# Performance work log

Hardware: AMD Instinct MI355X
Metric: run time of the kernel (lower is better)

## Reference

```python
import jax, jax.numpy as jnp
import numpy as np

B, SQ, SC, D = 16, 1024, 1024, 768
H = 2 * D  # 1536, fc width
NCLS = 2


def setup_inputs() -> dict:
    key = jax.random.key(0)
    ks = jax.random.split(key, 8)
    q = jax.random.normal(ks[0], (B, SQ, D), jnp.float32)
    c = jax.random.normal(ks[1], (B, SC, D), jnp.float32)
    mask_q = jax.random.randint(ks[2], (B, SQ), 0, 2).astype(jnp.int32)
    mask_c = jax.random.randint(ks[3], (B, SC), 0, 2).astype(jnp.int32)
    labels = jax.random.randint(ks[4], (B,), 0, NCLS)
    # torch nn.Linear convention: weight [out, in], y = x @ W.T + b
    W1 = jax.random.normal(ks[5], (H, H), jnp.float32) * 0.02
    b1 = jnp.zeros((H,), jnp.float32)
    W2 = jax.random.normal(ks[6], (NCLS, H), jnp.float32) * 0.02
    b2 = jnp.zeros((NCLS,), jnp.float32)
    return dict(q=q, c=c, mask_q=mask_q, mask_c=mask_c, labels=labels,
                W1=W1, b1=b1, W2=W2, b2=b2)


def reference(q, c, mask_q, mask_c, labels, W1, b1, W2, b2):
    # masked QK^T score matrix: [B, SQ, SC]
    s = jnp.einsum('bik,bjk->bij', q, c)
    s = s * mask_q[:, :, None].astype(s.dtype) * mask_c[:, None, :].astype(s.dtype)
    s = jnp.where(s == 0.0, -jnp.inf, s)  # x[x == 0.0] = -inf
    p = jnp.nan_to_num(jax.nn.softmax(s, axis=2))   # softmax over context axis
    pp = jnp.nan_to_num(jax.nn.softmax(s, axis=1))  # softmax over question axis
    a = jnp.einsum('bjk,bij->bk', c, p)   # weighted combine into context feats
    bb = jnp.einsum('bik,bij->bk', q, pp)  # weighted combine into question feats
    x = jnp.concatenate([a, bb], axis=1)  # [B, 1536]
    x = jnp.tanh(x @ W1.T + b1)           # fc1 + tanh (dropout = identity in eval)
    logits = x @ W2.T + b2                # fc2
    logp = jax.nn.log_softmax(logits, axis=1)  # LogSoftmax(dim=1)
    # NLLLoss (mean reduction)
    loss = -jnp.mean(jnp.take_along_axis(logp, labels[:, None], axis=1))
    return (loss, logp)
```

## Files before the change

### kernel.cpp

```cpp
#include <hip/hip_runtime.h>
#include <math.h>

#define B_   16
#define SQ_  1024
#define SC_  1024
#define D_   768
#define H_   1536
#define BK   32
#define LDK  40

typedef __attribute__((ext_vector_type(4))) float f32x4;
typedef __attribute__((ext_vector_type(8))) short bf16x8;

__device__ __forceinline__ unsigned cvtpk(float x, float y) {
  unsigned r;
  asm("v_cvt_pk_bf16_f32 %0, %1, %2" : "=v"(r) : "v"(x), "v"(y));
  return r;
}

__device__ __forceinline__ void split4(float4 v, uint2& hi, uint2& lo) {
  unsigned h01 = cvtpk(v.x, v.y);
  unsigned h23 = cvtpk(v.z, v.w);
  float h0 = __uint_as_float(h01 << 16);
  float h1 = __uint_as_float(h01 & 0xFFFF0000u);
  float h2 = __uint_as_float(h23 << 16);
  float h3 = __uint_as_float(h23 & 0xFFFF0000u);
  hi = make_uint2(h01, h23);
  lo = make_uint2(cvtpk(v.x - h0, v.y - h1), cvtpk(v.z - h2, v.w - h3));
}

__device__ __forceinline__ double exp_pos(float s) {
  float t = s * 1.4426950408889634f;
  float n = floorf(t);
  float p = exp2f(t - n);
  long long e = (long long)n;
  double scale = __longlong_as_double((unsigned long long)(e + 1023LL) << 52);
  return (double)p * scale;
}

__global__ __launch_bounds__(256) void compact_kernel(
    const int* __restrict__ mask_q, const int* __restrict__ mask_c,
    int* __restrict__ idx_q, int* __restrict__ idx_c, int* __restrict__ cnt)
{
  int which = blockIdx.x & 1;
  int b     = blockIdx.x >> 1;
  const int* m = (which ? mask_c : mask_q) + b * 1024;
  int* idx     = (which ? idx_c : idx_q) + b * 1024;

  __shared__ int tsum[256];
  int t = threadIdx.x;
  int v[4], s = 0;
#pragma unroll
  for (int e = 0; e < 4; ++e) { v[e] = (m[t * 4 + e] != 0) ? 1 : 0; s += v[e]; }
  tsum[t] = s;
  __syncthreads();
  for (int off = 1; off < 256; off <<= 1) {
    int add = (t >= off) ? tsum[t - off] : 0;
    __syncthreads();
    tsum[t] += add;
    __syncthreads();
  }
  int pos = tsum[t] - s;
#pragma unroll
  for (int e = 0; e < 4; ++e) {
    if (v[e]) idx[pos++] = t * 4 + e;
  }
  if (t == 255) cnt[b * 2 + which] = tsum[255];
}

__global__ void tile_setup_kernel(const int* __restrict__ cnt, int* __restrict__ tmeta)
{
  if (threadIdx.x == 0) {
    int off = 0;
    for (int b = 0; b < B_; ++b) {
      int ntq = (cnt[2 * b] + 63) >> 6;
      int ntc = (cnt[2 * b + 1] + 63) >> 6;
      tmeta[1 + b]  = off;
      tmeta[17 + b] = ntc;
      off += ntq * ntc;
    }
    tmeta[0]  = off;
    tmeta[33] = 0;
  }
}

__global__ __launch_bounds__(256) void gemm_mfma_kernel(
    const float* __restrict__ q, const float* __restrict__ c,
    const int* __restrict__ idx_q, const int* __restrict__ idx_c,
    const int* __restrict__ cnt, int* __restrict__ tmeta,
    float* __restrict__ S, double* __restrict__ R, double* __restrict__ C)
{
  __shared__ unsigned short Ah[2][64][LDK];
  __shared__ unsigned short Al[2][64][LDK];
  __shared__ unsigned short Bh[2][64][LDK];
  __shared__ unsigned short Bl[2][64][LDK];
  __shared__ int tidx_s;

  const int t    = threadIdx.x;
  const int lane = t & 63;
  const int w    = t >> 6;
  const int srow = t >> 2;
  const int kc   = (t & 3) * 4;
  const int fr   = lane & 15;
  const int fq   = lane >> 4;
  const int kg   = fq * 8;

  const int total = tmeta[0];

  while (true) {
    if (t == 0) tidx_s = atomicAdd(&tmeta[33], 1);
    __syncthreads();
    const int idx = tidx_s;
    if (idx >= total) break;

    int bb = 0;
#pragma unroll
    for (int k = 1; k < 16; ++k) bb += (idx >= tmeta[1 + k]) ? 1 : 0;
    const int rem = idx - tmeta[1 + bb];
    const int ntc = tmeta[17 + bb];
    const int ty  = rem / ntc;
    const int tx  = rem - ty * ntc;
    const int i0  = ty * 64, j0 = tx * 64;
    const int nq  = cnt[2 * bb], nc = cnt[2 * bb + 1];

    const int rq = idx_q[bb * 1024 + min(i0 + srow, nq - 1)];
    const int rc = idx_c[bb * 1024 + min(j0 + srow, nc - 1)];
    const float* qrowP = q + ((size_t)bb * SQ_ + rq) * D_;
    const float* crowP = c + ((size_t)bb * SC_ + rc) * D_;

    f32x4 acc[4] = {};

    float4 av0 = *(const float4*)(qrowP + kc);
    float4 av1 = *(const float4*)(qrowP + kc + 16);
    float4 bv0 = *(const float4*)(crowP + kc);
    float4 bv1 = *(const float4*)(crowP + kc + 16);
    {
      uint2 hi, lo;
      split4(av0, hi, lo); *(uint2*)&Ah[0][srow][kc]      = hi; *(uint2*)&Al[0][srow][kc]      = lo;
      split4(av1, hi, lo); *(uint2*)&Ah[0][srow][kc + 16] = hi; *(uint2*)&Al[0][srow][kc + 16] = lo;
      split4(bv0, hi, lo); *(uint2*)&Bh[0][srow][kc]      = hi; *(uint2*)&Bl[0][srow][kc]      = lo;
      split4(bv1, hi, lo); *(uint2*)&Bh[0][srow][kc + 16] = hi; *(uint2*)&Bl[0][srow][kc + 16] = lo;
    }
    __syncthreads();

    int cur = 0;
    for (int k0 = 0; k0 < D_; k0 += BK) {
      const int next = k0 + BK;
      const bool has_next = (next < D_);
      if (has_next) {
        av0 = *(const float4*)(qrowP + next + kc);
        av1 = *(const float4*)(qrowP + next + kc + 16);
        bv0 = *(const float4*)(crowP + next + kc);
        bv1 = *(const float4*)(crowP + next + kc + 16);
      }

      bf16x8 b_h = *reinterpret_cast<const bf16x8*>(&Bh[cur][w * 16 + fr][kg]);
      bf16x8 b_l = *reinterpret_cast<const bf16x8*>(&Bl[cur][w * 16 + fr][kg]);
#pragma unroll
      for (int m = 0; m < 4; ++m) {
        bf16x8 a_h = *reinterpret_cast<const bf16x8*>(&Ah[cur][m * 16 + fr][kg]);
        bf16x8 a_l = *reinterpret_cast<const bf16x8*>(&Al[cur][m * 16 + fr][kg]);
        acc[m] = __builtin_amdgcn_mfma_f32_16x16x32_bf16(a_h, b_h, acc[m], 0, 0, 0);
        acc[m] = __builtin_amdgcn_mfma_f32_16x16x32_bf16(a_h, b_l, acc[m], 0, 0, 0);
        acc[m] = __builtin_amdgcn_mfma_f32_16x16x32_bf16(a_l, b_h, acc[m], 0, 0, 0);
      }

      if (has_next) {
        int nxt = cur ^ 1;
        uint2 hi, lo;
        split4(av0, hi, lo); *(uint2*)&Ah[nxt][srow][kc]      = hi; *(uint2*)&Al[nxt][srow][kc]      = lo;
        split4(av1, hi, lo); *(uint2*)&Ah[nxt][srow][kc + 16] = hi; *(uint2*)&Al[nxt][srow][kc + 16] = lo;
        split4(bv0, hi, lo); *(uint2*)&Bh[nxt][srow][kc]      = hi; *(uint2*)&Bl[nxt][srow][kc]      = lo;
        split4(bv1, hi, lo); *(uint2*)&Bh[nxt][srow][kc + 16] = hi; *(uint2*)&Bl[nxt][srow][kc + 16] = lo;
      }
      __syncthreads();
      cur ^= 1;
    }

    double* rowAcc = reinterpret_cast<double*>(&Ah[0][0][0]);
    const int col = j0 + w * 16 + fr;
    const bool cok = (col < nc);
    double colSum = 0.0;
#pragma unroll
    for (int m = 0; m < 4; ++m) {
      int rbase = i0 + m * 16 + fq * 4;
      float* Sp = S + ((size_t)bb * SQ_ + rbase) * SC_ + col;
#pragma unroll
      for (int rr = 0; rr < 4; ++rr) {
        float v = acc[m][rr];
        bool valid = ((rbase + rr) < nq) && cok && (v != 0.f);
        Sp[(size_t)rr * SC_] = valid ? v : -INFINITY;
        double e = valid ? exp_pos(v) : 0.0;
        colSum += e;
        double rsum = e;
        rsum += __shfl_xor(rsum, 1);
        rsum += __shfl_xor(rsum, 2);
        rsum += __shfl_xor(rsum, 4);
        rsum += __shfl_xor(rsum, 8);
        if (fr == 0) rowAcc[w * 64 + m * 16 + fq * 4 + rr] = rsum;
      }
    }
    colSum += __shfl_xor(colSum, 16);
    colSum += __shfl_xor(colSum, 32);
    if (fq == 0 && cok) atomicAdd(&C[bb * SC_ + col], colSum);
    __syncthreads();
    if (t < 64) {
      double rs = rowAcc[t] + rowAcc[64 + t] + rowAcc[128 + t] + rowAcc[192 + t];
      if ((i0 + t) < nq && rs != 0.0) atomicAdd(&R[bb * SQ_ + i0 + t], rs);
    }
    __syncthreads();
  }
}

__global__ __launch_bounds__(1024) void pass2_kernel(
    const float* __restrict__ S, const int* __restrict__ cnt,
    const double* __restrict__ R, const double* __restrict__ C,
    float* __restrict__ cp, float* __restrict__ rpp)
{
  __shared__ float lnR_lds[SQ_];
  __shared__ float red[16][64];

  int b  = blockIdx.y;
  int j0 = blockIdx.x * 64;
  int nq_pad = (cnt[2 * b] + 63) & ~63;
  int nc_pad = (cnt[2 * b + 1] + 63) & ~63;
  if (j0 >= nc_pad) return;
  int t = threadIdx.x;

  if (t < nq_pad) {
    double Ri = R[b * SQ_ + t];
    lnR_lds[t] = (Ri > 0.0) ? (float)log(Ri) : INFINITY;
  }
  __syncthreads();

  int lane = t & 63, wv = t >> 6;
  int j = j0 + lane;
  double Cj = C[b * SC_ + j];
  float lnCj = (Cj > 0.0) ? (float)log(Cj) : INFINITY;

  int chunk = nq_pad >> 4;
  int i0 = wv * chunk;
  const float* Sb = S + ((size_t)b * SQ_ + i0) * SC_ + j;

  float cpAcc = 0.f;
  for (int ii = 0; ii < chunk; ++ii) {
    int i = i0 + ii;
    float v = Sb[(size_t)ii * SC_];
    cpAcc += __expf(v - lnR_lds[i]);
    float e2 = __expf(v - lnCj);
#pragma unroll
    for (int o = 32; o; o >>= 1) e2 += __shfl_xor(e2, o);
    if (lane == 0) atomicAdd(&rpp[b * SQ_ + i], e2);
  }

  red[wv][lane] = cpAcc;
  __syncthreads();
  if (t < 64) {
    float s = 0.f;
#pragma unroll
    for (int k = 0; k < 16; ++k) s += red[k][t];
    cp[b * SC_ + j0 + t] = s;
  }
}

__global__ __launch_bounds__(256) void combine_kernel(
    const float* __restrict__ q, const float* __restrict__ c,
    const int* __restrict__ idx_q, const int* __restrict__ idx_c,
    const int* __restrict__ cnt,
    const float* __restrict__ cp, const float* __restrict__ rpp,
    float* __restrict__ X)
{
  int jc = blockIdx.x;
  int op = blockIdx.y;
  int b  = blockIdx.z;
  int t  = threadIdx.x;

  int n = op ? cnt[2 * b] : cnt[2 * b + 1];
  const float* src = op ? (q + (size_t)b * SQ_ * D_) : (c + (size_t)b * SC_ * D_);
  const float* wv  = op ? (rpp + b * SQ_) : (cp + b * SC_);
  const int*   idx = (op ? idx_q : idx_c) + b * 1024;

  float a0 = 0.f, a1 = 0.f, a2 = 0.f;
  int je = min(jc * 32 + 32, n);
  for (int j = jc * 32; j < je; ++j) {
    float wj = wv[j];
    const float* r = src + (size_t)idx[j] * D_;
    a0 += wj * r[t];
    a1 += wj * r[t + 256];
    a2 += wj * r[t + 512];
  }
  float* xp = X + (size_t)b * H_ + op * D_;
  atomicAdd(&xp[t], a0);
  atomicAdd(&xp[t + 256], a1);
  atomicAdd(&xp[t + 512], a2);
}

__global__ __launch_bounds__(256) void fc1_kernel(
    const float* __restrict__ X, const float* __restrict__ W1,
    const float* __restrict__ b1, float* __restrict__ Y)
{
  int w = threadIdx.x >> 6, lane = threadIdx.x & 63;
  int h = blockIdx.x * 4 + w;
  const float4* wr = (const float4*)(W1 + (size_t)h * H_);
  float4 wv[6];
#pragma unroll
  for (int it = 0; it < 6; ++it) wv[it] = wr[it * 64 + lane];
  float bias = b1[h];

  for (int b = 0; b < B_; ++b) {
    const float4* x = (const float4*)(X + (size_t)b * H_);
    float accv = 0.f;
#pragma unroll
    for (int it = 0; it < 6; ++it) {
      float4 xv = x[it * 64 + lane];
      accv += xv.x * wv[it].x + xv.y * wv[it].y + xv.z * wv[it].z + xv.w * wv[it].w;
    }
#pragma unroll
    for (int o = 32; o; o >>= 1) accv += __shfl_xor(accv, o);
    if (lane == 0) Y[(size_t)b * H_ + h] = tanhf(accv + bias);
  }
}

__global__ __launch_bounds__(64) void fc2_loss_kernel(
    const float* __restrict__ Y, const float* __restrict__ W2,
    const float* __restrict__ b2, const int* __restrict__ labels,
    float* __restrict__ out)
{
  __shared__ float logp_s[B_][2];
  int t = threadIdx.x;
  if (t < 2 * B_) {
    int b = t >> 1, n = t & 1;
    const float* y = Y + (size_t)b * H_;
    const float* w = W2 + (size_t)n * H_;
    float accv = b2[n];
    for (int k = 0; k < H_; ++k) accv += y[k] * w[k];
    logp_s[b][n] = accv;
  }
  __syncthreads();
  if (t < B_) {
    float l0 = logp_s[t][0], l1 = logp_s[t][1];
    float m = fmaxf(l0, l1);
    float lse = m + logf(expf(l0 - m) + expf(l1 - m));
    logp_s[t][0] = l0 - lse;
    logp_s[t][1] = l1 - lse;
  }
  __syncthreads();
  if (t < 2 * B_) out[1 + t] = logp_s[t >> 1][t & 1];
  if (t == 0) {
    float loss = 0.f;
    for (int b = 0; b < B_; ++b) loss -= logp_s[b][labels[b]];
    out[0] = loss / (float)B_;
  }
}

extern "C" void kernel_launch(void* const* d_in, const int* in_sizes, int n_in,
                              void* d_out, int out_size, void* d_ws, size_t ws_size,
                              hipStream_t stream) {
  const float* q      = (const float*)d_in[0];
  const float* c      = (const float*)d_in[1];
  const int*   mask_q = (const int*)d_in[2];
  const int*   mask_c = (const int*)d_in[3];
  const int*   labels = (const int*)d_in[4];
  const float* W1     = (const float*)d_in[5];
  const float* b1     = (const float*)d_in[6];
  const float* W2     = (const float*)d_in[7];
  const float* b2     = (const float*)d_in[8];
  float* out = (float*)d_out;

  float*  ws   = (float*)d_ws;
  float*  S    = ws;
  double* R    = (double*)(ws + (size_t)B_ * SQ_ * SC_);
  double* C    = R + B_ * SQ_;
  float*  cp   = (float*)(C + B_ * SC_);
  float*  rpp  = cp + B_ * SC_;
  int*    cnt  = (int*)(rpp + B_ * SQ_);
  int*    tmeta = cnt + 2 * B_;
  int*    idx_q = tmeta + 34;
  int*    idx_c = idx_q + B_ * SQ_;
  float*  X    = ws;
  float*  Y    = ws + B_ * H_;

  (void)hipMemsetAsync((void*)R, 0, (size_t)(2 * B_ * SQ_) * sizeof(double)
                              + (size_t)(2 * B_ * SC_) * sizeof(float), stream);

  compact_kernel<<<2 * B_, 256, 0, stream>>>(mask_q, mask_c, idx_q, idx_c, cnt);
  tile_setup_kernel<<<1, 64, 0, stream>>>(cnt, tmeta);

  gemm_mfma_kernel<<<1024, 256, 0, stream>>>(q, c, idx_q, idx_c, cnt, tmeta, S, R, C);

  pass2_kernel<<<dim3(SC_ / 64, B_), 1024, 0, stream>>>(S, cnt, R, C, cp, rpp);

  (void)hipMemsetAsync((void*)X, 0, (size_t)B_ * H_ * sizeof(float), stream);
  combine_kernel<<<dim3(32, 2, B_), 256, 0, stream>>>(q, c, idx_q, idx_c, cnt,
                                                      cp, rpp, X);
  fc1_kernel<<<H_ / 4, 256, 0, stream>>>(X, W1, b1, Y);
  fc2_loss_kernel<<<1, 64, 0, stream>>>(Y, W2, b2, labels, out);
}
```

Baseline: 164.0 us.

## Replace LDS-staged persistent GEMM with register-direct 128x128 tiles per block

The score GEMM now drops shared-memory staging and the atomic persistent tile queue. Each block covers a 128x128 tile with four waves of 64x64 each, and every lane loads its MFMA fragments straight from global memory, splits them into bf16 hi/lo in registers and accumulates a 4x4 grid of MFMA tiles. Row and column exp-sums are reduced in registers before the atomics. This removes LDS traffic and __syncthreads at the cost of heavy register pressure, strided uncoalesced global loads, and a launch grid that now depends on tmeta. The host launch code (not shown) must size the grid to match.

```diff
diff --git a/kernel.cpp b/kernel.cpp
--- a/kernel.cpp
+++ b/kernel.cpp
@@ -6,8 +6,6 @@
 #define SC_  1024
 #define D_   768
 #define H_   1536
-#define BK   32
-#define LDK  40
 
 typedef __attribute__((ext_vector_type(4))) float f32x4;
 typedef __attribute__((ext_vector_type(8))) short bf16x8;
@@ -18,15 +16,22 @@
   return r;
 }
 
-__device__ __forceinline__ void split4(float4 v, uint2& hi, uint2& lo) {
-  unsigned h01 = cvtpk(v.x, v.y);
-  unsigned h23 = cvtpk(v.z, v.w);
-  float h0 = __uint_as_float(h01 << 16);
-  float h1 = __uint_as_float(h01 & 0xFFFF0000u);
-  float h2 = __uint_as_float(h23 << 16);
-  float h3 = __uint_as_float(h23 & 0xFFFF0000u);
-  hi = make_uint2(h01, h23);
-  lo = make_uint2(cvtpk(v.x - h0, v.y - h1), cvtpk(v.z - h2, v.w - h3));
+__device__ __forceinline__ void split8(float4 r0, float4 r1, bf16x8& h8, bf16x8& l8) {
+  unsigned h01 = cvtpk(r0.x, r0.y);
+  unsigned h23 = cvtpk(r0.z, r0.w);
+  unsigned h45 = cvtpk(r1.x, r1.y);
+  unsigned h67 = cvtpk(r1.z, r1.w);
+  float f0 = __uint_as_float(h01 << 16), f1 = __uint_as_float(h01 & 0xFFFF0000u);
+  float f2 = __uint_as_float(h23 << 16), f3 = __uint_as_float(h23 & 0xFFFF0000u);
+  float f4 = __uint_as_float(h45 << 16), f5 = __uint_as_float(h45 & 0xFFFF0000u);
+  float f6 = __uint_as_float(h67 << 16), f7 = __uint_as_float(h67 & 0xFFFF0000u);
+  unsigned l01 = cvtpk(r0.x - f0, r0.y - f1);
+  unsigned l23 = cvtpk(r0.z - f2, r0.w - f3);
+  unsigned l45 = cvtpk(r1.x - f4, r1.y - f5);
+  unsigned l67 = cvtpk(r1.z - f6, r1.w - f7);
+  union U { unsigned u[4]; bf16x8 v; };
+  U H; H.u[0] = h01; H.u[1] = h23; H.u[2] = h45; H.u[3] = h67; h8 = H.v;
+  U L; L.u[0] = l01; L.u[1] = l23; L.u[2] = l45; L.u[3] = l67; l8 = L.v;
 }
 
 __device__ __forceinline__ double exp_pos(float s) {
@@ -73,142 +78,152 @@
   if (threadIdx.x == 0) {
     int off = 0;
     for (int b = 0; b < B_; ++b) {
-      int ntq = (cnt[2 * b] + 63) >> 6;
-      int ntc = (cnt[2 * b + 1] + 63) >> 6;
+      int ntq = (cnt[2 * b] + 127) >> 7;
+      int ntc = (cnt[2 * b + 1] + 127) >> 7;
       tmeta[1 + b]  = off;
       tmeta[17 + b] = ntc;
       off += ntq * ntc;
     }
-    tmeta[0]  = off;
-    tmeta[33] = 0;
-  }
-}
-
-__global__ __launch_bounds__(256) void gemm_mfma_kernel(
+    tmeta[0] = off;
+  }
+}
+
+__global__ __launch_bounds__(256, 1) void gemm_mfma_kernel(
     const float* __restrict__ q, const float* __restrict__ c,
     const int* __restrict__ idx_q, const int* __restrict__ idx_c,
-    const int* __restrict__ cnt, int* __restrict__ tmeta,
+    const int* __restrict__ cnt, const int* __restrict__ tmeta,
     float* __restrict__ S, double* __restrict__ R, double* __restrict__ C)
 {
-  __shared__ unsigned short Ah[2][64][LDK];
-  __shared__ unsigned short Al[2][64][LDK];
-  __shared__ unsigned short Bh[2][64][LDK];
-  __shared__ unsigned short Bl[2][64][LDK];
-  __shared__ int tidx_s;
+  const int flat  = blockIdx.x;
+  const int total = tmeta[0];
+  if (flat >= total) return;
 
   const int t    = threadIdx.x;
   const int lane = t & 63;
   const int w    = t >> 6;
-  const int srow = t >> 2;
-  const int kc   = (t & 3) * 4;
-  const int fr   = lane & 15;
-  const int fq   = lane >> 4;
-  const int kg   = fq * 8;
-
-  const int total = tmeta[0];
-
-  while (true) {
-    if (t == 0) tidx_s = atomicAdd(&tmeta[33], 1);
-    __syncthreads();
-    const int idx = tidx_s;
-    if (idx >= total) break;
-
-    int bb = 0;
-#pragma unroll
-    for (int k = 1; k < 16; ++k) bb += (idx >= tmeta[1 + k]) ? 1 : 0;
-    const int rem = idx - tmeta[1 + bb];
-    const int ntc = tmeta[17 + bb];
-    const int ty  = rem / ntc;
-    const int tx  = rem - ty * ntc;
-    const int i0  = ty * 64, j0 = tx * 64;
-    const int nq  = cnt[2 * bb], nc = cnt[2 * bb + 1];
-
-    const int rq = idx_q[bb * 1024 + min(i0 + srow, nq - 1)];
-    const int rc = idx_c[bb * 1024 + min(j0 + srow, nc - 1)];
-    const float* qrowP = q + ((size_t)bb * SQ_ + rq) * D_;
-    const float* crowP = c + ((size_t)bb * SC_ + rc) * D_;
-
-    f32x4 acc[4] = {};
-
-    float4 av0 = *(const float4*)(qrowP + kc);
-    float4 av1 = *(const float4*)(qrowP + kc + 16);
-    float4 bv0 = *(const float4*)(crowP + kc);
-    float4 bv1 = *(const float4*)(crowP + kc + 16);
-    {
-      uint2 hi, lo;
-      split4(av0, hi, lo); *(uint2*)&Ah[0][srow][kc]      = hi; *(uint2*)&Al[0][srow][kc]      = lo;
-      split4(av1, hi, lo); *(uint2*)&Ah[0][srow][kc + 16] = hi; *(uint2*)&Al[0][srow][kc + 16] = lo;
-      split4(bv0, hi, lo); *(uint2*)&Bh[0][srow][kc]      = hi; *(uint2*)&Bl[0][srow][kc]      = lo;
-      split4(bv1, hi, lo); *(uint2*)&Bh[0][srow][kc + 16] = hi; *(uint2*)&Bl[0][srow][kc + 16] = lo;
+
+  int bb = 0;
+#pragma unroll
+  for (int k = 1; k < 16; ++k) bb += (flat >= tmeta[1 + k]) ? 1 : 0;
+  const int rem = flat - tmeta[1 + bb];
+  const int ntc = tmeta[17 + bb];
+  const int ty  = rem / ntc;
+  const int tx  = rem - ty * ntc;
+  const int nq  = cnt[2 * bb], nc = cnt[2 * bb + 1];
+
+  const int i0 = ty * 128 + (w >> 1) * 64;
+  const int j0 = tx * 128 + (w & 1) * 64;
+  if (i0 >= nq || j0 >= nc) return;
+
+  const int fr = lane & 15;
+  const int fq = lane >> 4;
+
+  const float* aP[4];
+  const float* bP[4];
+#pragma unroll
+  for (int m = 0; m < 4; ++m) {
+    int r = idx_q[bb * 1024 + min(i0 + m * 16 + fr, nq - 1)];
+    aP[m] = q + ((size_t)bb * SQ_ + r) * D_ + fq * 8;
+  }
+#pragma unroll
+  for (int n = 0; n < 4; ++n) {
+    int cc = idx_c[bb * 1024 + min(j0 + n * 16 + fr, nc - 1)];
+    bP[n] = c + ((size_t)bb * SC_ + cc) * D_ + fq * 8;
+  }
+
+  f32x4 acc[4][4] = {};
+  float4 aRaw[4][2], bRaw[4][2];
+#pragma unroll
+  for (int m = 0; m < 4; ++m) {
+    aRaw[m][0] = *(const float4*)(aP[m]);
+    aRaw[m][1] = *(const float4*)(aP[m] + 4);
+  }
+#pragma unroll
+  for (int n = 0; n < 4; ++n) {
+    bRaw[n][0] = *(const float4*)(bP[n]);
+    bRaw[n][1] = *(const float4*)(bP[n] + 4);
+  }
+
+  for (int k0 = 0; k0 < D_; k0 += 32) {
+    bf16x8 aH[4], aL[4], bH[4], bL[4];
+#pragma unroll
+    for (int m = 0; m < 4; ++m) split8(aRaw[m][0], aRaw[m][1], aH[m], aL[m]);
+#pragma unroll
+    for (int n = 0; n < 4; ++n) split8(bRaw[n][0], bRaw[n][1], bH[n], bL[n]);
+
+    const int nk = k0 + 32;
+    if (nk < D_) {
+#pragma unroll
+      for (int m = 0; m < 4; ++m) {
+        aRaw[m][0] = *(const float4*)(aP[m] + nk);
+        aRaw[m][1] = *(const float4*)(aP[m] + nk + 4);
+      }
+#pragma unroll
+      for (int n = 0; n < 4; ++n) {
+        bRaw[n][0] = *(const float4*)(bP[n] + nk);
+        bRaw[n][1] = *(const float4*)(bP[n] + nk + 4);
+      }
     }
-    __syncthreads();
-
-    int cur = 0;
-    for (int k0 = 0; k0 < D_; k0 += BK) {
-      const int next = k0 + BK;
-      const bool has_next = (next < D_);
-      if (has_next) {
-        av0 = *(const float4*)(qrowP + next + kc);
-        av1 = *(const float4*)(qrowP + next + kc + 16);
-        bv0 = *(const float4*)(crowP + next + kc);
-        bv1 = *(const float4*)(crowP + next + kc + 16);
+
+#pragma unroll
+    for (int n = 0; n < 4; ++n)
+#pragma unroll
+      for (int m = 0; m < 4; ++m) {
+        acc[m][n] = __builtin_amdgcn_mfma_f32_16x16x32_bf16(aH[m], bH[n], acc[m][n], 0, 0, 0);
+        acc[m][n] = __builtin_amdgcn_mfma_f32_16x16x32_bf16(aH[m], bL[n], acc[m][n], 0, 0, 0);
+        acc[m][n] = __builtin_amdgcn_mfma_f32_16x16x32_bf16(aL[m], bH[n], acc[m][n], 0, 0, 0);
       }
-
-      bf16x8 b_h = *reinterpret_cast<const bf16x8*>(&Bh[cur][w * 16 + fr][kg]);
-      bf16x8 b_l = *reinterpret_cast<const bf16x8*>(&Bl[cur][w * 16 + fr][kg]);
-#pragma unroll
-      for (int m = 0; m < 4; ++m) {
-        bf16x8 a_h = *reinterpret_cast<const bf16x8*>(&Ah[cur][m * 16 + fr][kg]);
-        bf16x8 a_l = *reinterpret_cast<const bf16x8*>(&Al[cur][m * 16 + fr][kg]);
-        acc[m] = __builtin_amdgcn_mfma_f32_16x16x32_bf16(a_h, b_h, acc[m], 0, 0, 0);
-        acc[m] = __builtin_amdgcn_mfma_f32_16x16x32_bf16(a_h, b_l, acc[m], 0, 0, 0);
-        acc[m] = __builtin_amdgcn_mfma_f32_16x16x32_bf16(a_l, b_h, acc[m], 0, 0, 0);
-      }
-
-      if (has_next) {
-        int nxt = cur ^ 1;
-        uint2 hi, lo;
-        split4(av0, hi, lo); *(uint2*)&Ah[nxt][srow][kc]      = hi; *(uint2*)&Al[nxt][srow][kc]      = lo;
-        split4(av1, hi, lo); *(uint2*)&Ah[nxt][srow][kc + 16] = hi; *(uint2*)&Al[nxt][srow][kc + 16] = lo;
-        split4(bv0, hi, lo); *(uint2*)&Bh[nxt][srow][kc]      = hi; *(uint2*)&Bl[nxt][srow][kc]      = lo;
-        split4(bv1, hi, lo); *(uint2*)&Bh[nxt][srow][kc + 16] = hi; *(uint2*)&Bl[nxt][srow][kc + 16] = lo;
-      }
-      __syncthreads();
-      cur ^= 1;
-    }
-
-    double* rowAcc = reinterpret_cast<double*>(&Ah[0][0][0]);
-    const int col = j0 + w * 16 + fr;
-    const bool cok = (col < nc);
-    double colSum = 0.0;
-#pragma unroll
-    for (int m = 0; m < 4; ++m) {
-      int rbase = i0 + m * 16 + fq * 4;
+  }
+
+  double rowPart[4][4];
+#pragma unroll
+  for (int m = 0; m < 4; ++m)
+#pragma unroll
+    for (int rr = 0; rr < 4; ++rr) rowPart[m][rr] = 0.0;
+  double colSum[4] = {0.0, 0.0, 0.0, 0.0};
+
+#pragma unroll
+  for (int m = 0; m < 4; ++m) {
+    const int rbase = i0 + m * 16 + fq * 4;
+#pragma unroll
+    for (int n = 0; n < 4; ++n) {
+      const int col = j0 + n * 16 + fr;
+      const bool cok = (col < nc);
       float* Sp = S + ((size_t)bb * SQ_ + rbase) * SC_ + col;
 #pragma unroll
       for (int rr = 0; rr < 4; ++rr) {
-        float v = acc[m][rr];
+        float v = acc[m][n][rr];
         bool valid = ((rbase + rr) < nq) && cok && (v != 0.f);
         Sp[(size_t)rr * SC_] = valid ? v : -INFINITY;
         double e = valid ? exp_pos(v) : 0.0;
-        colSum += e;
-        double rsum = e;
-        rsum += __shfl_xor(rsum, 1);
-        rsum += __shfl_xor(rsum, 2);
-        rsum += __shfl_xor(rsum, 4);
-        rsum += __shfl_xor(rsum, 8);
-        if (fr == 0) rowAcc[w * 64 + m * 16 + fq * 4 + rr] = rsum;
+        colSum[n] += e;
+        rowPart[m][rr] += e;
       }
     }
-    colSum += __shfl_xor(colSum, 16);
-    colSum += __shfl_xor(colSum, 32);
-    if (fq == 0 && cok) atomicAdd(&C[bb * SC_ + col], colSum);
-    __syncthreads();
-    if (t < 64) {
-      double rs = rowAcc[t] + rowAcc[64 + t] + rowAcc[128 + t] + rowAcc[192 + t];
-      if ((i0 + t) < nq && rs != 0.0) atomicAdd(&R[bb * SQ_ + i0 + t], rs);
+  }
+#pragma unroll
+  for (int m = 0; m < 4; ++m)
+#pragma unroll
+    for (int rr = 0; rr < 4; ++rr) {
+      double x = rowPart[m][rr];
+      x += __shfl_xor(x, 1); x += __shfl_xor(x, 2);
+      x += __shfl_xor(x, 4); x += __shfl_xor(x, 8);
+      rowPart[m][rr] = x;
     }
-    __syncthreads();
+  if (fr == 0) {
+#pragma unroll
+    for (int m = 0; m < 4; ++m)
+#pragma unroll
+      for (int rr = 0; rr < 4; ++rr) {
+        double x = rowPart[m][rr];
+        if (x != 0.0) atomicAdd(&R[bb * SQ_ + i0 + m * 16 + fq * 4 + rr], x);
+      }
+  }
+#pragma unroll
+  for (int n = 0; n < 4; ++n) {
+    double x = colSum[n];
+    x += __shfl_xor(x, 16); x += __shfl_xor(x, 32);
+    if (fq == 0 && x != 0.0) atomicAdd(&C[bb * SC_ + j0 + n * 16 + fr], x);
   }
 }
 
```

Result: slower. 203.2 us (+23.9%).

## Fold memsets into compact kernel and replace persistent tile scheduler with 3D grid

Applied to the files above, without the earlier changes.

Zeroing of the R/C/cp/rpp accumulators and the X buffer now happens inside compact_kernel instead of two hipMemsetAsync calls. The separate tile_setup kernel and the atomic-counter persistent loop are gone: the GEMM uses a 3D grid covering every 64x64 tile per batch, and tiles past the compacted counts exit at once. Row sums are now reduced with shuffles and added to R with per-row atomics directly, which removes the LDS staging and its extra barriers. In exchange there are more atomics on R and many empty blocks launched. X moves to its own workspace region so it no longer aliases S.

```diff
diff --git a/kernel.cpp b/kernel.cpp
--- a/kernel.cpp
+++ b/kernel.cpp
@@ -40,15 +40,20 @@
 
 __global__ __launch_bounds__(256) void compact_kernel(
     const int* __restrict__ mask_q, const int* __restrict__ mask_c,
-    int* __restrict__ idx_q, int* __restrict__ idx_c, int* __restrict__ cnt)
+    int* __restrict__ idx_q, int* __restrict__ idx_c, int* __restrict__ cnt,
+    float* __restrict__ zeroA, int lenA, float* __restrict__ zeroB, int lenB)
 {
   int which = blockIdx.x & 1;
   int b     = blockIdx.x >> 1;
   const int* m = (which ? mask_c : mask_q) + b * 1024;
   int* idx     = (which ? idx_c : idx_q) + b * 1024;
 
+  int t = threadIdx.x;
+  int gid = blockIdx.x * 256 + t;
+  for (int i = gid; i < lenA; i += 32 * 256) zeroA[i] = 0.f;
+  for (int i = gid; i < lenB; i += 32 * 256) zeroB[i] = 0.f;
+
   __shared__ int tsum[256];
-  int t = threadIdx.x;
   int v[4], s = 0;
 #pragma unroll
   for (int e = 0; e < 4; ++e) { v[e] = (m[t * 4 + e] != 0) ? 1 : 0; s += v[e]; }
@@ -68,147 +73,127 @@
   if (t == 255) cnt[b * 2 + which] = tsum[255];
 }
 
-__global__ void tile_setup_kernel(const int* __restrict__ cnt, int* __restrict__ tmeta)
-{
-  if (threadIdx.x == 0) {
-    int off = 0;
-    for (int b = 0; b < B_; ++b) {
-      int ntq = (cnt[2 * b] + 63) >> 6;
-      int ntc = (cnt[2 * b + 1] + 63) >> 6;
-      tmeta[1 + b]  = off;
-      tmeta[17 + b] = ntc;
-      off += ntq * ntc;
-    }
-    tmeta[0]  = off;
-    tmeta[33] = 0;
-  }
-}
-
 __global__ __launch_bounds__(256) void gemm_mfma_kernel(
     const float* __restrict__ q, const float* __restrict__ c,
     const int* __restrict__ idx_q, const int* __restrict__ idx_c,
-    const int* __restrict__ cnt, int* __restrict__ tmeta,
+    const int* __restrict__ cnt,
     float* __restrict__ S, double* __restrict__ R, double* __restrict__ C)
 {
   __shared__ unsigned short Ah[2][64][LDK];
   __shared__ unsigned short Al[2][64][LDK];
   __shared__ unsigned short Bh[2][64][LDK];
   __shared__ unsigned short Bl[2][64][LDK];
-  __shared__ int tidx_s;
+
+  const int bb = blockIdx.z;
+  const int i0 = blockIdx.y * 64;
+  const int j0 = blockIdx.x * 64;
+  const int nq = cnt[2 * bb], nc = cnt[2 * bb + 1];
+  if (i0 >= nq || j0 >= nc) return;
 
   const int t    = threadIdx.x;
   const int lane = t & 63;
   const int w    = t >> 6;
+
   const int srow = t >> 2;
   const int kc   = (t & 3) * 4;
   const int fr   = lane & 15;
   const int fq   = lane >> 4;
   const int kg   = fq * 8;
 
-  const int total = tmeta[0];
-
-  while (true) {
-    if (t == 0) tidx_s = atomicAdd(&tmeta[33], 1);
+  const int rq = idx_q[bb * 1024 + min(i0 + srow, nq - 1)];
+  const int rc = idx_c[bb * 1024 + min(j0 + srow, nc - 1)];
+  const float* qrowP = q + ((size_t)bb * SQ_ + rq) * D_;
+  const float* crowP = c + ((size_t)bb * SC_ + rc) * D_;
+
+  f32x4 acc[4] = {};
+
+  float4 av0 = *(const float4*)(qrowP + kc);
+  float4 av1 = *(const float4*)(qrowP + kc + 16);
+  float4 bv0 = *(const float4*)(crowP + kc);
+  float4 bv1 = *(const float4*)(crowP + kc + 16);
+  {
+    uint2 hi, lo;
+    split4(av0, hi, lo); *(uint2*)&Ah[0][srow][kc]      = hi; *(uint2*)&Al[0][srow][kc]      = lo;
+    split4(av1, hi, lo); *(uint2*)&Ah[0][srow][kc + 16] = hi; *(uint2*)&Al[0][srow][kc + 16] = lo;
+    split4(bv0, hi, lo); *(uint2*)&Bh[0][srow][kc]      = hi; *(uint2*)&Bl[0][srow][kc]      = lo;
+    split4(bv1, hi, lo); *(uint2*)&Bh[0][srow][kc + 16] = hi; *(uint2*)&Bl[0][srow][kc + 16] = lo;
+  }
+  __syncthreads();
+
+  int cur = 0;
+  for (int k0 = 0; k0 < D_; k0 += BK) {
+    const int next = k0 + BK;
+    const bool has_next = (next < D_);
+    if (has_next) {
+      av0 = *(const float4*)(qrowP + next + kc);
+      av1 = *(const float4*)(qrowP + next + kc + 16);
+      bv0 = *(const float4*)(crowP + next + kc);
+      bv1 = *(const float4*)(crowP + next + kc + 16);
+    }
+
+    bf16x8 b_h = *reinterpret_cast<const bf16x8*>(&Bh[cur][w * 16 + fr][kg]);
+    bf16x8 b_l = *reinterpret_cast<const bf16x8*>(&Bl[cur][w * 16 + fr][kg]);
+#pragma unroll
+    for (int m = 0; m < 4; ++m) {
+      bf16x8 a_h = *reinterpret_cast<const bf16x8*>(&Ah[cur][m * 16 + fr][kg]);
+      bf16x8 a_l = *reinterpret_cast<const bf16x8*>(&Al[cur][m * 16 + fr][kg]);
+      acc[m] = __builtin_amdgcn_mfma_f32_16x16x32_bf16(a_h, b_h, acc[m], 0, 0, 0);
+      acc[m] = __builtin_amdgcn_mfma_f32_16x16x32_bf16(a_h, b_l, acc[m], 0, 0, 0);
+      acc[m] = __builtin_amdgcn_mfma_f32_16x16x32_bf16(a_l, b_h, acc[m], 0, 0, 0);
+    }
+
+    if (has_next) {
+      int nxt = cur ^ 1;
+      uint2 hi, lo;
+      split4(av0, hi, lo); *(uint2*)&Ah[nxt][srow][kc]      = hi; *(uint2*)&Al[nxt][srow][kc]      = lo;
+      split4(av1, hi, lo); *(uint2*)&Ah[nxt][srow][kc + 16] = hi; *(uint2*)&Al[nxt][srow][kc + 16] = lo;
+      split4(bv0, hi, lo); *(uint2*)&Bh[nxt][srow][kc]      = hi; *(uint2*)&Bl[nxt][srow][kc]      = lo;
+      split4(bv1, hi, lo); *(uint2*)&Bh[nxt][srow][kc + 16] = hi; *(uint2*)&Bl[nxt][srow][kc + 16] = lo;
+    }
     __syncthreads();
-    const int idx = tidx_s;
-    if (idx >= total) break;
-
-    int bb = 0;
-#pragma unroll
-    for (int k = 1; k < 16; ++k) bb += (idx >= tmeta[1 + k]) ? 1 : 0;
-    const int rem = idx - tmeta[1 + bb];
-    const int ntc = tmeta[17 + bb];
-    const int ty  = rem / ntc;
-    const int tx  = rem - ty * ntc;
-    const int i0  = ty * 64, j0 = tx * 64;
-    const int nq  = cnt[2 * bb], nc = cnt[2 * bb + 1];
-
-    const int rq = idx_q[bb * 1024 + min(i0 + srow, nq - 1)];
-    const int rc = idx_c[bb * 1024 + min(j0 + srow, nc - 1)];
-    const float* qrowP = q + ((size_t)bb * SQ_ + rq) * D_;
-    const float* crowP = c + ((size_t)bb * SC_ + rc) * D_;
-
-    f32x4 acc[4] = {};
-
-    float4 av0 = *(const float4*)(qrowP + kc);
-    float4 av1 = *(const float4*)(qrowP + kc + 16);
-    float4 bv0 = *(const float4*)(crowP + kc);
-    float4 bv1 = *(const float4*)(crowP + kc + 16);
-    {
-      uint2 hi, lo;
-      split4(av0, hi, lo); *(uint2*)&Ah[0][srow][kc]      = hi; *(uint2*)&Al[0][srow][kc]      = lo;
-      split4(av1, hi, lo); *(uint2*)&Ah[0][srow][kc + 16] = hi; *(uint2*)&Al[0][srow][kc + 16] = lo;
-      split4(bv0, hi, lo); *(uint2*)&Bh[0][srow][kc]      = hi; *(uint2*)&Bl[0][srow][kc]      = lo;
-      split4(bv1, hi, lo); *(uint2*)&Bh[0][srow][kc + 16] = hi; *(uint2*)&Bl[0][srow][kc + 16] = lo;
-    }
-    __syncthreads();
-
-    int cur = 0;
-    for (int k0 = 0; k0 < D_; k0 += BK) {
-      const int next = k0 + BK;
-      const bool has_next = (next < D_);
-      if (has_next) {
-        av0 = *(const float4*)(qrowP + next + kc);
-        av1 = *(const float4*)(qrowP + next + kc + 16);
-        bv0 = *(const float4*)(crowP + next + kc);
-        bv1 = *(const float4*)(crowP + next + kc + 16);
+    cur ^= 1;
+  }
+
+  const int col = j0 + w * 16 + fr;
+  const bool cok = (col < nc);
+  double rowPart[4][4];
+  double colSum = 0.0;
+#pragma unroll
+  for (int m = 0; m < 4; ++m) {
+    const int rbase = i0 + m * 16 + fq * 4;
+    float* Sp = S + ((size_t)bb * SQ_ + rbase) * SC_ + col;
+#pragma unroll
+    for (int rr = 0; rr < 4; ++rr) {
+      float v = acc[m][rr];
+      bool valid = ((rbase + rr) < nq) && cok && (v != 0.f);
+      Sp[(size_t)rr * SC_] = valid ? v : -INFINITY;
+      double e = valid ? exp_pos(v) : 0.0;
+      colSum += e;
+      rowPart[m][rr] = e;
+    }
+  }
+#pragma unroll
+  for (int m = 0; m < 4; ++m)
+#pragma unroll
+    for (int rr = 0; rr < 4; ++rr) {
+      double x = rowPart[m][rr];
+      x += __shfl_xor(x, 1); x += __shfl_xor(x, 2);
+      x += __shfl_xor(x, 4); x += __shfl_xor(x, 8);
+      rowPart[m][rr] = x;
+    }
+  if (fr == 0) {
+#pragma unroll
+    for (int m = 0; m < 4; ++m)
+#pragma unroll
+      for (int rr = 0; rr < 4; ++rr) {
+        double x = rowPart[m][rr];
+        if (x != 0.0) atomicAdd(&R[bb * SQ_ + i0 + m * 16 + fq * 4 + rr], x);
       }
-
-      bf16x8 b_h = *reinterpret_cast<const bf16x8*>(&Bh[cur][w * 16 + fr][kg]);
-      bf16x8 b_l = *reinterpret_cast<const bf16x8*>(&Bl[cur][w * 16 + fr][kg]);
-#pragma unroll
-      for (int m = 0; m < 4; ++m) {
-        bf16x8 a_h = *reinterpret_cast<const bf16x8*>(&Ah[cur][m * 16 + fr][kg]);
-        bf16x8 a_l = *reinterpret_cast<const bf16x8*>(&Al[cur][m * 16 + fr][kg]);
-        acc[m] = __builtin_amdgcn_mfma_f32_16x16x32_bf16(a_h, b_h, acc[m], 0, 0, 0);
-        acc[m] = __builtin_amdgcn_mfma_f32_16x16x32_bf16(a_h, b_l, acc[m], 0, 0, 0);
-        acc[m] = __builtin_amdgcn_mfma_f32_16x16x32_bf16(a_l, b_h, acc[m], 0, 0, 0);
-      }
-
-      if (has_next) {
-        int nxt = cur ^ 1;
-        uint2 hi, lo;
-        split4(av0, hi, lo); *(uint2*)&Ah[nxt][srow][kc]      = hi; *(uint2*)&Al[nxt][srow][kc]      = lo;
-        split4(av1, hi, lo); *(uint2*)&Ah[nxt][srow][kc + 16] = hi; *(uint2*)&Al[nxt][srow][kc + 16] = lo;
-        split4(bv0, hi, lo); *(uint2*)&Bh[nxt][srow][kc]      = hi; *(uint2*)&Bl[nxt][srow][kc]      = lo;
-        split4(bv1, hi, lo); *(uint2*)&Bh[nxt][srow][kc + 16] = hi; *(uint2*)&Bl[nxt][srow][kc + 16] = lo;
-      }
-      __syncthreads();
-      cur ^= 1;
-    }
-
-    double* rowAcc = reinterpret_cast<double*>(&Ah[0][0][0]);
-    const int col = j0 + w * 16 + fr;
-    const bool cok = (col < nc);
-    double colSum = 0.0;
-#pragma unroll
-    for (int m = 0; m < 4; ++m) {
-      int rbase = i0 + m * 16 + fq * 4;
-      float* Sp = S + ((size_t)bb * SQ_ + rbase) * SC_ + col;
-#pragma unroll
-      for (int rr = 0; rr < 4; ++rr) {
-        float v = acc[m][rr];
-        bool valid = ((rbase + rr) < nq) && cok && (v != 0.f);
-        Sp[(size_t)rr * SC_] = valid ? v : -INFINITY;
-        double e = valid ? exp_pos(v) : 0.0;
-        colSum += e;
-        double rsum = e;
-        rsum += __shfl_xor(rsum, 1);
-        rsum += __shfl_xor(rsum, 2);
-        rsum += __shfl_xor(rsum, 4);
-        rsum += __shfl_xor(rsum, 8);
-        if (fr == 0) rowAcc[w * 64 + m * 16 + fq * 4 + rr] = rsum;
-      }
-    }
-    colSum += __shfl_xor(colSum, 16);
-    colSum += __shfl_xor(colSum, 32);
-    if (fq == 0 && cok) atomicAdd(&C[bb * SC_ + col], colSum);
-    __syncthreads();
-    if (t < 64) {
-      double rs = rowAcc[t] + rowAcc[64 + t] + rowAcc[128 + t] + rowAcc[192 + t];
-      if ((i0 + t) < nq && rs != 0.0) atomicAdd(&R[bb * SQ_ + i0 + t], rs);
-    }
-    __syncthreads();
+  }
+  {
+    double x = colSum;
+    x += __shfl_xor(x, 16); x += __shfl_xor(x, 32);
+    if (fq == 0 && cok && x != 0.0) atomicAdd(&C[bb * SC_ + col], x);
   }
 }
 
@@ -367,30 +352,29 @@
   const float* b2     = (const float*)d_in[8];
   float* out = (float*)d_out;
 
-  float*  ws   = (float*)d_ws;
-  float*  S    = ws;
-  double* R    = (double*)(ws + (size_t)B_ * SQ_ * SC_);
-  double* C    = R + B_ * SQ_;
-  float*  cp   = (float*)(C + B_ * SC_);
-  float*  rpp  = cp + B_ * SC_;
-  int*    cnt  = (int*)(rpp + B_ * SQ_);
-  int*    tmeta = cnt + 2 * B_;
-  int*    idx_q = tmeta + 34;
+  float*  ws    = (float*)d_ws;
+  float*  S     = ws;
+  double* R     = (double*)(ws + (size_t)B_ * SQ_ * SC_);
+  double* C     = R + B_ * SQ_;
+  float*  cp    = (float*)(C + B_ * SC_);
+  float*  rpp   = cp + B_ * SC_;
+  int*    cnt   = (int*)(rpp + B_ * SQ_);
+  int*    idx_q = cnt + 2 * B_;
   int*    idx_c = idx_q + B_ * SQ_;
-  float*  X    = ws;
-  float*  Y    = ws + B_ * H_;
-
-  (void)hipMemsetAsync((void*)R, 0, (size_t)(2 * B_ * SQ_) * sizeof(double)
-                              + (size_t)(2 * B_ * SC_) * sizeof(float), stream);
-
-  compact_kernel<<<2 * B_, 256, 0, stream>>>(mask_q, mask_c, idx_q, idx_c, cnt);
-  tile_setup_kernel<<<1, 64, 0, stream>>>(cnt, tmeta);
-
-  gemm_mfma_kernel<<<1024, 256, 0, stream>>>(q, c, idx_q, idx_c, cnt, tmeta, S, R, C);
+  float*  X     = (float*)(idx_c + B_ * SC_);
+  float*  Y     = X + B_ * H_;
+  float*  zeroA = (float*)R;
+  const int lenA = 2 * B_ * SQ_ * 2 + 2 * B_ * SC_;
+  const int lenB = B_ * H_;
+
+  compact_kernel<<<2 * B_, 256, 0, stream>>>(mask_q, mask_c, idx_q, idx_c, cnt,
+                                             zeroA, lenA, X, lenB);
+
+  dim3 g1(SC_ / 64, SQ_ / 64, B_);
+  gemm_mfma_kernel<<<g1, 256, 0, stream>>>(q, c, idx_q, idx_c, cnt, S, R, C);
 
   pass2_kernel<<<dim3(SC_ / 64, B_), 1024, 0, stream>>>(S, cnt, R, C, cp, rpp);
 
-  (void)hipMemsetAsync((void*)X, 0, (size_t)B_ * H_ * sizeof(float), stream);
   combine_kernel<<<dim3(32, 2, B_), 256, 0, stream>>>(q, c, idx_q, idx_c, cnt,
                                                       cp, rpp, X);
   fc1_kernel<<<H_ / 4, 256, 0, stream>>>(X, W1, b1, Y);
```

After: 180.5 us. 1.1x slower.
